# Optimization experiments

Measured on AMD Instinct MI355X. Metric: run time of the kernel, lower is better.

## Reference

```python
import jax, jax.numpy as jnp
import numpy as np
from jax import lax

B, CIN, COUT, CS, K, KSZ, L = 64, 256, 256, 256, 4, 3, 1024
HIDDEN = CS // 4          # ratio = 4
TEMPERATURE = 30.0


def setup_inputs() -> dict:
    key = jax.random.key(0)
    k0, k1, k2, k3, k4, k5 = jax.random.split(key, 6)
    x = jax.random.normal(k0, (B, CIN, L, 1), dtype=jnp.float32)
    cond = jax.random.normal(k1, (B, CS), dtype=jnp.float32)
    # attention MLP (1x1 convs == dense layers on (B, C))
    w1 = jax.random.normal(k2, (HIDDEN, CS), dtype=jnp.float32) * (2.0 / CS) ** 0.5
    w2 = jax.random.normal(k3, (K, HIDDEN), dtype=jnp.float32) * (2.0 / HIDDEN) ** 0.5
    # K expert kernels and biases
    weight = jax.random.normal(k4, (K, COUT, CIN, KSZ, KSZ), dtype=jnp.float32) * 0.05
    bias = jax.random.normal(k5, (K, COUT), dtype=jnp.float32) * 0.05
    return {"x": x, "cond": cond, "w1": w1, "w2": w2, "weight": weight, "bias": bias}


def reference(x, cond, w1, w2, weight, bias):
    # Attention routing: softmax over K mixture logits (temperature-scaled)
    logits = jax.nn.relu(cond @ w1.T) @ w2.T          # (B, K)
    att = jax.nn.softmax(logits / TEMPERATURE, axis=-1)
    # Per-sample aggregated kernel / bias (mixture of K experts)
    agg_w = jnp.einsum('bk,koihw->boihw', att, weight)  # (B, COUT, CIN, 3, 3)
    agg_b = att @ bias                                  # (B, COUT)
    # Per-sample conv2d (stride 1, padding 1) — vmap replaces the groups=B trick
    def conv_one(xi, wi):
        y = lax.conv_general_dilated(
            xi[None], wi, window_strides=(1, 1), padding=[(1, 1), (1, 1)],
            dimension_numbers=('NCHW', 'OIHW', 'NCHW'))
        return y[0]
    out = jax.vmap(conv_one)(x, agg_w)                  # (B, COUT, L, 1)
    return out + agg_b[:, :, None, None]
```

## Files before the change

### kernel.cpp

```cpp
#include <hip/hip_runtime.h>

typedef __attribute__((ext_vector_type(8))) short bf16x8;
typedef __attribute__((ext_vector_type(4))) short s16x4;
typedef __attribute__((ext_vector_type(4))) float f32x4;

#define B_SZ   64
#define CIN    256
#define COUT   256
#define CS     256
#define HIDDEN 64
#define L_SZ   1024
#define LPAD   1026
#define TEMP   30.0f

#define OFF_ATT   0u
#define OFF_AGGB  1024u
#define OFF_WAGG  66560u
#define OFF_XBF   25232384u

__device__ __forceinline__ unsigned short f2bf(float f) {
    union { float f; unsigned int u; } v; v.f = f;
    unsigned int u = v.u;
    return (unsigned short)((u + 0x7fffu + ((u >> 16) & 1u)) >> 16);
}

__device__ __forceinline__ void load_lds16(const unsigned short* g, unsigned short* l) {
    __builtin_amdgcn_global_load_lds(
        (const __attribute__((address_space(1))) unsigned int*)g,
        (__attribute__((address_space(3))) unsigned int*)l, 16, 0, 0);
}

__global__ void routing_kernel(const float* __restrict__ cond,
                               const float* __restrict__ w1,
                               const float* __restrict__ w2,
                               const float* __restrict__ bias,
                               float* __restrict__ att_g,
                               float* __restrict__ aggb_g,
                               unsigned short* __restrict__ xbf) {
    __shared__ float cond_s[CS];
    __shared__ float h_s[HIDDEN];
    __shared__ float lg_s[4];
    int t = threadIdx.x;
    int b = blockIdx.x;
    cond_s[t] = cond[b * CS + t];
    xbf[(size_t)b * LPAD * CIN + t] = 0;
    xbf[((size_t)b * LPAD + (LPAD - 1)) * CIN + t] = 0;
    __syncthreads();
    int jj = t >> 2, s = t & 3;
    float p = 0.f;
    const float* w1r = w1 + jj * CS + s * 64;
    const float* cs  = cond_s + s * 64;
    #pragma unroll 16
    for (int c = 0; c < 64; ++c) p += cs[c] * w1r[c];
    p += __shfl_down(p, 2, 4);
    p += __shfl_down(p, 1, 4);
    if (s == 0) h_s[jj] = fmaxf(p, 0.f);
    __syncthreads();
    if (t < 4) {
        float z = 0.f;
        #pragma unroll 16
        for (int h = 0; h < HIDDEN; ++h) z += h_s[h] * w2[t * HIDDEN + h];
        lg_s[t] = z * (1.0f / TEMP);
    }
    __syncthreads();
    float l0 = lg_s[0], l1 = lg_s[1], l2 = lg_s[2], l3 = lg_s[3];
    float mx = fmaxf(fmaxf(l0, l1), fmaxf(l2, l3));
    float e0 = __expf(l0 - mx), e1 = __expf(l1 - mx);
    float e2 = __expf(l2 - mx), e3 = __expf(l3 - mx);
    float inv = 1.0f / (e0 + e1 + e2 + e3);
    float a0 = e0 * inv, a1 = e1 * inv, a2 = e2 * inv, a3 = e3 * inv;
    if (t == 0) {
        att_g[b * 4 + 0] = a0; att_g[b * 4 + 1] = a1;
        att_g[b * 4 + 2] = a2; att_g[b * 4 + 3] = a3;
    }
    aggb_g[b * COUT + t] = a0 * bias[0 * COUT + t] + a1 * bias[1 * COUT + t]
                         + a2 * bias[2 * COUT + t] + a3 * bias[3 * COUT + t];
}

__global__ void xpose_kernel(const float* __restrict__ x,
                             unsigned short* __restrict__ xbf) {
    __shared__ unsigned short tileB[64 * 68];
    int lt = blockIdx.x, it = blockIdx.y, b = blockIdx.z;
    int t = threadIdx.x;
    int w = t >> 6, lane = t & 63;
    int sub = lane & 15, grp = lane >> 4;

    const float4* xp4 = (const float4*)x;
    #pragma unroll
    for (int j = 0; j < 4; ++j) {
        int i_loc = w * 16 + j * 4 + grp;
        float4 v = xp4[((size_t)(b * CIN + it * 64 + i_loc)) * (L_SZ / 4)
                       + lt * 16 + sub];
        {
            float a = (grp & 1) ? v.x : v.y;
            float c = (grp & 1) ? v.z : v.w;
            float ra = __shfl_xor(a, 16);
            float rc = __shfl_xor(c, 16);
            if (grp & 1) { v.x = ra; v.z = rc; } else { v.y = ra; v.w = rc; }
        }
        {
            float a  = (grp & 2) ? v.x : v.z;
            float b2 = (grp & 2) ? v.y : v.w;
            float ra = __shfl_xor(a, 32);
            float rb = __shfl_xor(b2, 32);
            if (grp & 2) { v.x = ra; v.y = rb; } else { v.z = ra; v.w = rb; }
        }
        int l_loc = sub * 4 + grp;
        s16x4 pk;
        pk.x = (short)f2bf(v.x); pk.y = (short)f2bf(v.y);
        pk.z = (short)f2bf(v.z); pk.w = (short)f2bf(v.w);
        *(s16x4*)&tileB[l_loc * 68 + w * 16 + j * 4] = pk;
    }
    __syncthreads();
    int row = t >> 2, c0 = t & 3;
    unsigned short* dst = xbf + ((size_t)b * LPAD + lt * 64 + row + 1) * CIN + it * 64;
    #pragma unroll
    for (int h = 0; h < 2; ++h) {
        int c = c0 + h * 4;
        bf16x8 vv = *(const bf16x8*)&tileB[row * 68 + c * 8];
        *(bf16x8*)&dst[c * 8] = vv;
    }
}

__global__ void wagg_kernel(const float* __restrict__ weight,
                            const float* __restrict__ att_g,
                            unsigned short* __restrict__ wagg) {
    __shared__ float w_s[4][2304];
    __shared__ float att_s[128];
    int o = blockIdx.x, bc = blockIdx.y;
    int t = threadIdx.x;
    if (t < 128) att_s[t] = att_g[bc * 128 + t];
    #pragma unroll
    for (int k = 0; k < 4; ++k) {
        const float4* src = (const float4*)(weight + ((size_t)k * COUT + o) * 2304);
        for (int idx = t; idx < 576; idx += 256)
            *(float4*)&w_s[k][idx * 4] = src[idx];
    }
    __syncthreads();
    int i = t;
    float wv[3][4];
    #pragma unroll
    for (int kh = 0; kh < 3; ++kh)
        #pragma unroll
        for (int k = 0; k < 4; ++k)
            wv[kh][k] = w_s[k][i * 9 + kh * 3 + 1];
    for (int bb = 0; bb < 32; ++bb) {
        int b = bc * 32 + bb;
        float a0 = att_s[bb * 4 + 0], a1 = att_s[bb * 4 + 1];
        float a2 = att_s[bb * 4 + 2], a3 = att_s[bb * 4 + 3];
        #pragma unroll
        for (int kh = 0; kh < 3; ++kh) {
            float v = wv[kh][0] * a0 + wv[kh][1] * a1 + wv[kh][2] * a2 + wv[kh][3] * a3;
            wagg[(((size_t)b * 3 + kh) * COUT + o) * CIN + i] = f2bf(v);
        }
    }
}

__global__ __launch_bounds__(256)
void dynconv_gemm(const unsigned short* __restrict__ wagg,
                  const unsigned short* __restrict__ xbf,
                  const float* __restrict__ aggb,
                  float* __restrict__ out) {
    __shared__ unsigned short As[3 * 128 * 32];
    __shared__ unsigned short Bs[144 * 32];
    int bx = blockIdx.x;
    int r8 = bx & 7, s = bx >> 3;
    int tile = s & 15, q = s >> 4;
    int b = r8 + 8 * q;
    int mt = tile & 1, nt = tile >> 1;
    int l0 = nt * 128, m0 = mt * 128;
    int t = threadIdx.x;
    int w = t >> 6, lane = t & 63;
    int ln = lane & 15, hi = lane >> 4;
    int wm = w & 1, wn = w >> 1;
    int jq = lane >> 2, jc = lane & 3;
    int gc = jc ^ ((jq >> 1) & 3);

    f32x4 acc[4][4];
    #pragma unroll
    for (int a = 0; a < 4; ++a)
        #pragma unroll
        for (int c = 0; c < 4; ++c) acc[a][c] = (f32x4){0.f, 0.f, 0.f, 0.f};

    const unsigned short* wb = wagg + (size_t)b * 3 * COUT * CIN;
    const unsigned short* xb = xbf + (size_t)b * LPAD * CIN;

    for (int it = 0; it < 8; ++it) {
        int i0 = it * 32;
        #pragma unroll
        for (int si = 0; si < 6; ++si) {
            int inst = w * 6 + si;
            int R = inst * 16 + jq;
            int kh = R >> 7, m = R & 127;
            const unsigned short* g =
                wb + ((size_t)(kh * COUT + m0 + m)) * CIN + i0 + gc * 8;
            load_lds16(g, &As[inst * 512]);
        }
        for (int bi = w; bi < 9; bi += 4) {
            int r = bi * 16 + jq;
            if (r < 130) {
                const unsigned short* g = xb + (size_t)(l0 + r) * CIN + i0 + gc * 8;
                load_lds16(g, &Bs[bi * 512]);
            }
        }
        __syncthreads();
        #pragma unroll
        for (int kh = 0; kh < 3; ++kh) {
            bf16x8 af[4], bfr[4];
            #pragma unroll
            for (int mi = 0; mi < 4; ++mi) {
                int m = wm * 64 + mi * 16 + ln;
                af[mi] = *(const bf16x8*)&As[kh * 4096 + m * 32 + (hi ^ ((m >> 1) & 3)) * 8];
            }
            #pragma unroll
            for (int ni = 0; ni < 4; ++ni) {
                int r = wn * 64 + ni * 16 + ln + kh;
                bfr[ni] = *(const bf16x8*)&Bs[r * 32 + (hi ^ ((r >> 1) & 3)) * 8];
            }
            #pragma unroll
            for (int mi = 0; mi < 4; ++mi)
                #pragma unroll
                for (int ni = 0; ni < 4; ++ni)
                    acc[mi][ni] = __builtin_amdgcn_mfma_f32_16x16x32_bf16(
                        af[mi], bfr[ni], acc[mi][ni], 0, 0, 0);
        }
        __syncthreads();
    }

    const float* abb = aggb + b * COUT;
    float* ob = out + (size_t)b * COUT * L_SZ;
    #pragma unroll
    for (int mi = 0; mi < 4; ++mi) {
        #pragma unroll
        for (int reg = 0; reg < 4; ++reg) {
            int o = m0 + wm * 64 + mi * 16 + hi * 4 + reg;
            float bv = abb[o];
            #pragma unroll
            for (int ni = 0; ni < 4; ++ni) {
                int l = l0 + wn * 64 + ni * 16 + ln;
                ob[(size_t)o * L_SZ + l] = acc[mi][ni][reg] + bv;
            }
        }
    }
}

extern "C" void kernel_launch(void* const* d_in, const int* in_sizes, int n_in,
                              void* d_out, int out_size, void* d_ws, size_t ws_size,
                              hipStream_t stream) {
    const float* x      = (const float*)d_in[0];
    const float* cond   = (const float*)d_in[1];
    const float* w1     = (const float*)d_in[2];
    const float* w2     = (const float*)d_in[3];
    const float* weight = (const float*)d_in[4];
    const float* bias   = (const float*)d_in[5];
    float* out = (float*)d_out;
    char* ws = (char*)d_ws;
    float* att_g  = (float*)(ws + OFF_ATT);
    float* aggb_g = (float*)(ws + OFF_AGGB);
    unsigned short* wagg = (unsigned short*)(ws + OFF_WAGG);
    unsigned short* xbf  = (unsigned short*)(ws + OFF_XBF);

    routing_kernel<<<64, 256, 0, stream>>>(cond, w1, w2, bias, att_g, aggb_g, xbf);
    xpose_kernel<<<dim3(16, 4, 64), 256, 0, stream>>>(x, xbf);
    wagg_kernel<<<dim3(256, 2), 256, 0, stream>>>(weight, att_g, wagg);
    dynconv_gemm<<<1024, 256, 0, stream>>>(wagg, xbf, aggb_g, out);
}
```

Measured before the change: 175.2 us.

## Widen stores in transpose, weight aggregation and GEMM epilogue via LDS staging

The transpose kernel now covers all 256 input channels in one block and writes full 512-byte rows to the bf16 buffer. The weight-aggregation kernel drops the batch split: each block loads the expert weights once and each thread writes two packed bf16 values. The GEMM epilogue stages the fp32 accumulators plus bias through shared memory so each output row is written with coalesced 16-byte stores, and launch bounds request 4 blocks per CU. These aim to cut uncoalesced and narrow global writes, at the cost of extra shared memory, more barriers and a larger LDS tile in the transpose.

```diff
diff --git a/kernel.cpp b/kernel.cpp
--- a/kernel.cpp
+++ b/kernel.cpp
@@ -77,48 +77,46 @@
                          + a2 * bias[2 * COUT + t] + a3 * bias[3 * COUT + t];
 }
 
-__global__ void xpose_kernel(const float* __restrict__ x,
-                             unsigned short* __restrict__ xbf) {
-    __shared__ unsigned short tileB[64 * 68];
-    int lt = blockIdx.x, it = blockIdx.y, b = blockIdx.z;
+__global__ __launch_bounds__(256)
+void xpose_kernel(const float* __restrict__ x,
+                  unsigned short* __restrict__ xbf) {
+    __shared__ __align__(16) unsigned short tile[64 * 264];
+    int lt = blockIdx.x, b = blockIdx.y;
     int t = threadIdx.x;
     int w = t >> 6, lane = t & 63;
     int sub = lane & 15, grp = lane >> 4;
-
     const float4* xp4 = (const float4*)x;
     #pragma unroll
-    for (int j = 0; j < 4; ++j) {
-        int i_loc = w * 16 + j * 4 + grp;
-        float4 v = xp4[((size_t)(b * CIN + it * 64 + i_loc)) * (L_SZ / 4)
-                       + lt * 16 + sub];
-        {
-            float a = (grp & 1) ? v.x : v.y;
-            float c = (grp & 1) ? v.z : v.w;
-            float ra = __shfl_xor(a, 16);
-            float rc = __shfl_xor(c, 16);
-            if (grp & 1) { v.x = ra; v.z = rc; } else { v.y = ra; v.w = rc; }
-        }
-        {
-            float a  = (grp & 2) ? v.x : v.z;
-            float b2 = (grp & 2) ? v.y : v.w;
-            float ra = __shfl_xor(a, 32);
-            float rb = __shfl_xor(b2, 32);
-            if (grp & 2) { v.x = ra; v.y = rb; } else { v.z = ra; v.w = rb; }
-        }
-        int l_loc = sub * 4 + grp;
-        s16x4 pk;
-        pk.x = (short)f2bf(v.x); pk.y = (short)f2bf(v.y);
-        pk.z = (short)f2bf(v.z); pk.w = (short)f2bf(v.w);
-        *(s16x4*)&tileB[l_loc * 68 + w * 16 + j * 4] = pk;
-    }
-    __syncthreads();
-    int row = t >> 2, c0 = t & 3;
-    unsigned short* dst = xbf + ((size_t)b * LPAD + lt * 64 + row + 1) * CIN + it * 64;
-    #pragma unroll
-    for (int h = 0; h < 2; ++h) {
-        int c = c0 + h * 4;
-        bf16x8 vv = *(const bf16x8*)&tileB[row * 68 + c * 8];
-        *(bf16x8*)&dst[c * 8] = vv;
+    for (int it = 0; it < 4; ++it) {
+        #pragma unroll
+        for (int j = 0; j < 4; ++j) {
+            int i_loc = it * 64 + w * 16 + j * 4 + grp;
+            float4 v = xp4[((size_t)(b * CIN + i_loc)) * (L_SZ / 4) + lt * 16 + sub];
+            { float a = (grp & 1) ? v.x : v.y;
+              float c = (grp & 1) ? v.z : v.w;
+              float ra = __shfl_xor(a, 16);
+              float rc = __shfl_xor(c, 16);
+              if (grp & 1) { v.x = ra; v.z = rc; } else { v.y = ra; v.w = rc; } }
+            { float a  = (grp & 2) ? v.x : v.z;
+              float b2 = (grp & 2) ? v.y : v.w;
+              float ra = __shfl_xor(a, 32);
+              float rb = __shfl_xor(b2, 32);
+              if (grp & 2) { v.x = ra; v.y = rb; } else { v.z = ra; v.w = rb; } }
+            int l_loc = sub * 4 + grp;
+            s16x4 pk;
+            pk.x = (short)f2bf(v.x); pk.y = (short)f2bf(v.y);
+            pk.z = (short)f2bf(v.z); pk.w = (short)f2bf(v.w);
+            *(s16x4*)&tile[l_loc * 264 + it * 64 + w * 16 + j * 4] = pk;
+        }
+    }
+    __syncthreads();
+    int half = lane >> 5, c16 = lane & 31;
+    unsigned short* dstb = xbf + ((size_t)b * LPAD + lt * 64 + 1) * CIN;
+    #pragma unroll
+    for (int rr = 0; rr < 16; rr += 2) {
+        int row = w * 16 + rr + half;
+        bf16x8 vv = *(const bf16x8*)&tile[row * 264 + c16 * 8];
+        *(bf16x8*)&dstb[(size_t)row * CIN + c16 * 8] = vv;
     }
 }
 
@@ -126,10 +124,10 @@
                             const float* __restrict__ att_g,
                             unsigned short* __restrict__ wagg) {
     __shared__ float w_s[4][2304];
-    __shared__ float att_s[128];
-    int o = blockIdx.x, bc = blockIdx.y;
-    int t = threadIdx.x;
-    if (t < 128) att_s[t] = att_g[bc * 128 + t];
+    __shared__ float att_s[256];
+    int o = blockIdx.x;
+    int t = threadIdx.x;
+    att_s[t] = att_g[t];
     #pragma unroll
     for (int k = 0; k < 4; ++k) {
         const float4* src = (const float4*)(weight + ((size_t)k * COUT + o) * 2304);
@@ -137,32 +135,39 @@
             *(float4*)&w_s[k][idx * 4] = src[idx];
     }
     __syncthreads();
-    int i = t;
-    float wv[3][4];
+    int i2 = (t & 127) * 2, half = t >> 7;
+    float wv[3][2][4];
     #pragma unroll
     for (int kh = 0; kh < 3; ++kh)
         #pragma unroll
-        for (int k = 0; k < 4; ++k)
-            wv[kh][k] = w_s[k][i * 9 + kh * 3 + 1];
-    for (int bb = 0; bb < 32; ++bb) {
-        int b = bc * 32 + bb;
+        for (int d = 0; d < 2; ++d)
+            #pragma unroll
+            for (int k = 0; k < 4; ++k)
+                wv[kh][d][k] = w_s[k][(i2 + d) * 9 + kh * 3 + 1];
+    for (int bb = half * 32; bb < half * 32 + 32; ++bb) {
         float a0 = att_s[bb * 4 + 0], a1 = att_s[bb * 4 + 1];
         float a2 = att_s[bb * 4 + 2], a3 = att_s[bb * 4 + 3];
         #pragma unroll
         for (int kh = 0; kh < 3; ++kh) {
-            float v = wv[kh][0] * a0 + wv[kh][1] * a1 + wv[kh][2] * a2 + wv[kh][3] * a3;
-            wagg[(((size_t)b * 3 + kh) * COUT + o) * CIN + i] = f2bf(v);
-        }
-    }
-}
-
-__global__ __launch_bounds__(256)
+            float v0 = wv[kh][0][0] * a0 + wv[kh][0][1] * a1
+                     + wv[kh][0][2] * a2 + wv[kh][0][3] * a3;
+            float v1 = wv[kh][1][0] * a0 + wv[kh][1][1] * a1
+                     + wv[kh][1][2] * a2 + wv[kh][1][3] * a3;
+            ushort2 pk; pk.x = f2bf(v0); pk.y = f2bf(v1);
+            *(ushort2*)&wagg[(((size_t)bb * 3 + kh) * COUT + o) * CIN + i2] = pk;
+        }
+    }
+}
+
+__global__ __launch_bounds__(256, 4)
 void dynconv_gemm(const unsigned short* __restrict__ wagg,
                   const unsigned short* __restrict__ xbf,
                   const float* __restrict__ aggb,
                   float* __restrict__ out) {
-    __shared__ unsigned short As[3 * 128 * 32];
-    __shared__ unsigned short Bs[144 * 32];
+    __shared__ __align__(16) unsigned char smem[33792];
+    unsigned short* As = (unsigned short*)smem;
+    unsigned short* Bs = (unsigned short*)(smem + 24576);
+    float* Cs = (float*)smem;
     int bx = blockIdx.x;
     int r8 = bx & 7, s = bx >> 3;
     int tile = s & 15, q = s >> 4;
@@ -230,16 +235,28 @@
     const float* abb = aggb + b * COUT;
     float* ob = out + (size_t)b * COUT * L_SZ;
     #pragma unroll
-    for (int mi = 0; mi < 4; ++mi) {
-        #pragma unroll
-        for (int reg = 0; reg < 4; ++reg) {
-            int o = m0 + wm * 64 + mi * 16 + hi * 4 + reg;
-            float bv = abb[o];
-            #pragma unroll
-            for (int ni = 0; ni < 4; ++ni) {
-                int l = l0 + wn * 64 + ni * 16 + ln;
-                ob[(size_t)o * L_SZ + l] = acc[mi][ni][reg] + bv;
-            }
+    for (int p = 0; p < 2; ++p) {
+        __syncthreads();
+        if (wm == p) {
+            #pragma unroll
+            for (int mi = 0; mi < 4; ++mi)
+                #pragma unroll
+                for (int reg = 0; reg < 4; ++reg) {
+                    int r = mi * 16 + hi * 4 + reg;
+                    float bv = abb[m0 + p * 64 + r];
+                    #pragma unroll
+                    for (int ni = 0; ni < 4; ++ni)
+                        Cs[r * 132 + wn * 64 + ni * 16 + ln] = acc[mi][ni][reg] + bv;
+                }
+        }
+        __syncthreads();
+        #pragma unroll
+        for (int v = 0; v < 8; ++v) {
+            int idx4 = v * 256 + t;
+            int row = idx4 >> 5;
+            int c4 = idx4 & 31;
+            f32x4 val = *(const f32x4*)&Cs[row * 132 + c4 * 4];
+            *(f32x4*)&ob[(size_t)(m0 + p * 64 + row) * L_SZ + l0 + c4 * 4] = val;
         }
     }
 }
@@ -261,7 +278,7 @@
     unsigned short* xbf  = (unsigned short*)(ws + OFF_XBF);
 
     routing_kernel<<<64, 256, 0, stream>>>(cond, w1, w2, bias, att_g, aggb_g, xbf);
-    xpose_kernel<<<dim3(16, 4, 64), 256, 0, stream>>>(x, xbf);
-    wagg_kernel<<<dim3(256, 2), 256, 0, stream>>>(weight, att_g, wagg);
+    xpose_kernel<<<dim3(16, 64), 256, 0, stream>>>(x, xbf);
+    wagg_kernel<<<256, 256, 0, stream>>>(weight, att_g, wagg);
     dynconv_gemm<<<1024, 256, 0, stream>>>(wagg, xbf, aggb_g, out);
 }
```

Measured after the change: 179.8 us. 2.6% more time.
